# Optimization experiments

Measured on AMD Instinct MI355X. Metric: run time of the kernel, lower is better.

The kernel has to match this reference:

```python
import jax, jax.numpy as jnp
import numpy as np

# NF4 16-level codebook (bitsandbytes values)
NF4_CODEBOOK = jnp.array([
    -1.0, -0.6961928009986877, -0.5250730514526367, -0.39491748809814453,
    -0.28444138169288635, -0.18477343022823334, -0.09105003625154495, 0.0,
    0.07958029955625534, 0.16093020141124725, 0.24611230194568634,
    0.33791524171829224, 0.44070982933044434, 0.5626170039176941,
    0.7229568362236328, 1.0], dtype=jnp.float32)

GROUP = 64      # quant_group_size for NF4
R = 16          # LoRA rank
ALPHA = 16      # lora_alpha -> scaling = ALPHA / R = 1.0
E, H, I, T, TOPK = 8, 2048, 1024, 512, 2


def nf4_dequant_gkn(packed, scales, K, N):
    """packed: [E, K//2, N] uint8-valued ints (two 4-bit codes per byte along K).
    scales: [E, K//GROUP, N] float32 per-group absmax. Returns [E, K, N] fp32."""
    e = packed.shape[0]
    lo = packed & 15
    hi = (packed >> 4) & 15
    codes = jnp.stack([lo, hi], axis=2).reshape(e, K, N)      # interleave along K
    w = NF4_CODEBOOK[codes]                                    # [E, K, N]
    w = w.reshape(e, K // GROUP, GROUP, N) * scales[:, :, None, :]
    return w.reshape(e, K, N)


def setup_inputs() -> dict:
    key = jax.random.key(0)
    ks = jax.random.split(key, 16)
    lora_std = 1.0 / np.sqrt(H)
    return {
        "x": jax.random.normal(ks[0], (T, H), jnp.float32),
        "topk_idx": jax.random.randint(ks[1], (T, TOPK), 0, E, jnp.int32),
        "topk_w": jax.random.uniform(ks[2], (T, TOPK), jnp.float32),
        "gate_packed": jax.random.randint(ks[3], (E, H // 2, I), 0, 256, jnp.int32),
        "gate_scales": jax.random.uniform(ks[4], (E, H // GROUP, I), jnp.float32) * 0.02,
        "up_packed": jax.random.randint(ks[5], (E, H // 2, I), 0, 256, jnp.int32),
        "up_scales": jax.random.uniform(ks[6], (E, H // GROUP, I), jnp.float32) * 0.02,
        "down_packed": jax.random.randint(ks[7], (E, I // 2, H), 0, 256, jnp.int32),
        "down_scales": jax.random.uniform(ks[8], (E, I // GROUP, H), jnp.float32) * 0.02,
        "gate_A": jax.random.normal(ks[9], (E, H, R), jnp.float32) * lora_std,
        "gate_B": jax.random.normal(ks[10], (E, R, I), jnp.float32) * 0.02,
        "up_A": jax.random.normal(ks[11], (E, H, R), jnp.float32) * lora_std,
        "up_B": jax.random.normal(ks[12], (E, R, I), jnp.float32) * 0.02,
        "down_A": jax.random.normal(ks[13], (E, I, R), jnp.float32) * lora_std,
        "down_B": jax.random.normal(ks[14], (E, R, H), jnp.float32) * 0.02,
    }


def reference(x, topk_idx, topk_w, gate_packed, gate_scales, up_packed, up_scales,
              down_packed, down_scales, gate_A, gate_B, up_A, up_B, down_A, down_B):
    scaling = ALPHA / R
    # Dequantized NF4 base + LoRA delta, GKN layout [E, K, N]
    Wg = nf4_dequant_gkn(gate_packed, gate_scales, H, I) + scaling * jnp.einsum('ekr,ern->ekn', gate_A, gate_B)
    Wu = nf4_dequant_gkn(up_packed, up_scales, H, I) + scaling * jnp.einsum('ekr,ern->ekn', up_A, up_B)
    Wd = nf4_dequant_gkn(down_packed, down_scales, I, H) + scaling * jnp.einsum('ekr,ern->ekn', down_A, down_B)
    # Grouped GEMM (dense-over-experts reference): SwiGLU per expert
    g = jnp.einsum('th,ehi->eti', x, Wg)          # [E, T, I]
    u = jnp.einsum('th,ehi->eti', x, Wu)
    h = jax.nn.silu(g) * u
    o = jnp.einsum('eti,eih->eth', h, Wd)         # [E, T, H]
    # Routing combine: per-token per-expert weight from top-k assignments
    w_te = jnp.sum((topk_idx[:, :, None] == jnp.arange(E)) * topk_w[:, :, None], axis=1)  # [T, E]
    return jnp.einsum('eth,te->th', o, w_te)
```

## Files before the change

### kernel.cpp

```cpp
#include <hip/hip_runtime.h>
#include <math.h>

#define NE 8
#define NH 2048
#define NI 1024
#define NT 512
#define NTOPK 2
#define NR 16
#define NGROUP 64
#define NPAIR (NT*NTOPK)

#define SPG 1040
#define SPD 528

typedef short bf16x8 __attribute__((ext_vector_type(8)));
typedef float f32x16 __attribute__((ext_vector_type(16)));
typedef unsigned int u32;

#define MFMA32 __builtin_amdgcn_mfma_f32_32x32x16_bf16

__device__ const float NF4_TAB[16] = {
    -1.0f, -0.6961928009986877f, -0.5250730514526367f, -0.39491748809814453f,
    -0.28444138169288635f, -0.18477343022823334f, -0.09105003625154495f, 0.0f,
    0.07958029955625534f, 0.16093020141124725f, 0.24611230194568634f,
    0.33791524171829224f, 0.44070982933044434f, 0.5626170039176941f,
    0.7229568362236328f, 1.0f};

#define OFF_EXPOFF 0
#define OFF_TOK    256
#define OFF_EXP    4352
#define OFF_W      8448
#define OFF_XAG    12544
#define OFF_XAU    45312
#define OFF_HA     78080
#define OFF_XCT    131072
#define OFF_GU     4325376
#define OFF_HT     10616832
#define OFF_CG     12713984
#define OFF_CU     21233664
#define OFF_CD     29753344

__device__ inline u32 f2bf(float f) {
    return (__float_as_uint(f) + 0x8000u) >> 16;
}
__device__ inline u32 bfpack2(float a, float b) {
    return ((__float_as_uint(a) + 0x8000u) >> 16) |
           ((__float_as_uint(b) + 0x8000u) & 0xFFFF0000u);
}
__device__ inline bf16x8 asbf(uint4 w) {
    union { uint4 u; bf16x8 b; } c; c.u = w; return c.b;
}
__device__ inline bf16x8 bfzero() { return asbf(make_uint4(0,0,0,0)); }
__device__ inline float bf2f(u32 v) { return __uint_as_float(v << 16); }

__device__ __forceinline__ void stage16(const void* g, void* l) {
    __builtin_amdgcn_global_load_lds(
        (const __attribute__((address_space(1))) u32*)g,
        (__attribute__((address_space(3))) u32*)l, 16, 0, 0);
}
#define WAITV0()  asm volatile("s_waitcnt vmcnt(0)" ::: "memory")

__global__ __launch_bounds__(256) void k_cmp3(const u32* __restrict__ gin,
                                              const u32* __restrict__ uin,
                                              const u32* __restrict__ din,
                                              unsigned char* __restrict__ cg,
                                              unsigned char* __restrict__ cu,
                                              unsigned char* __restrict__ cd) {
    __shared__ unsigned char tile[32][33];
    int z = blockIdx.z;
    const u32* in; unsigned char* out; int K2, N, SP, e;
    if (z < 2 * NE) {
        e = z >> 1;
        in = (z & 1) ? uin : gin; out = (z & 1) ? cu : cg;
        K2 = NH / 2; N = NI; SP = SPG;
    } else {
        e = z - 2 * NE;
        in = din; out = cd;
        K2 = NI / 2; N = NH; SP = SPD;
    }
    int kp0 = blockIdx.y * 32, c0 = blockIdx.x * 32;
    if (kp0 >= K2 || c0 >= N) return;
    const u32* ip = in + (size_t)e * K2 * N + (size_t)kp0 * N + c0;
    int tid = threadIdx.x;
    int r = tid >> 5, c = tid & 31;
    #pragma unroll
    for (int i = 0; i < 4; ++i)
        tile[r + 8 * i][c] = (unsigned char)ip[(size_t)(r + 8 * i) * N + c];
    __syncthreads();
    int col = tid >> 3, seg = tid & 7;
    u32 w = (u32)tile[seg * 4 + 0][col] | ((u32)tile[seg * 4 + 1][col] << 8) |
            ((u32)tile[seg * 4 + 2][col] << 16) |
            ((u32)tile[seg * 4 + 3][col] << 24);
    *(u32*)(out + (size_t)e * N * SP + (size_t)(c0 + col) * SP + kp0 + seg * 4) = w;
}

__global__ __launch_bounds__(1024) void k_route(const int* __restrict__ idx,
                                                const float* __restrict__ w,
                                                int* expert_off, int* ptok,
                                                int* pexp, float* pw) {
    __shared__ int cnt[NE], off[NE + 1], cur[NE];
    int tid = threadIdx.x;
    if (tid < NE) cnt[tid] = 0;
    __syncthreads();
    int e = idx[tid];
    float wt = w[tid];
    int t = tid >> 1;
    atomicAdd(&cnt[e], 1);
    __syncthreads();
    if (tid == 0) {
        off[0] = 0;
        for (int i = 0; i < NE; i++) off[i + 1] = off[i] + cnt[i];
    }
    __syncthreads();
    if (tid < NE) cur[tid] = off[tid];
    __syncthreads();
    int pos = atomicAdd(&cur[e], 1);
    ptok[pos] = t; pexp[pos] = e; pw[pos] = wt;
    if (tid <= NE) expert_off[tid] = off[tid];
}

__global__ __launch_bounds__(256) void k_xA(const float* __restrict__ x,
                                            const float* __restrict__ gA,
                                            const float* __restrict__ uA,
                                            const int* __restrict__ ptok,
                                            const int* __restrict__ pexp,
                                            unsigned short* __restrict__ xcT,
                                            unsigned short* __restrict__ xAg,
                                            unsigned short* __restrict__ xAu) {
    __shared__ float xs[NH];
    __shared__ float red[2][64][17];
    int p = blockIdx.x;
    int t = ptok[p], e = pexp[p];
    int tid = threadIdx.x;

    int k = tid * 8;
    const float* xr = x + (size_t)t * NH + k;
    float4 v0 = *(const float4*)xr;
    float4 v1 = *(const float4*)(xr + 4);
    uint4 w;
    w.x = bfpack2(v0.x, v0.y); w.y = bfpack2(v0.z, v0.w);
    w.z = bfpack2(v1.x, v1.y); w.w = bfpack2(v1.z, v1.w);
    *(uint4*)(xcT + ((size_t)(k >> 3) * NPAIR + p) * 8) = w;
    *(float4*)(xs + k) = v0;
    *(float4*)(xs + k + 4) = v1;
    __syncthreads();

    int ch = tid & 63, rg = tid >> 6;
    const float* gAr = gA + (size_t)e * NH * NR + rg * 4;
    const float* uAr = uA + (size_t)e * NH * NR + rg * 4;
    float4 sg = make_float4(0.f, 0.f, 0.f, 0.f);
    float4 su = make_float4(0.f, 0.f, 0.f, 0.f);
    #pragma unroll 4
    for (int jj = 0; jj < NH / 64; ++jj) {
        int j = jj * 64 + ch;
        float xv = xs[j];
        float4 ga = *(const float4*)(gAr + (size_t)j * NR);
        float4 ua = *(const float4*)(uAr + (size_t)j * NR);
        sg.x += xv * ga.x; sg.y += xv * ga.y; sg.z += xv * ga.z; sg.w += xv * ga.w;
        su.x += xv * ua.x; su.y += xv * ua.y; su.z += xv * ua.z; su.w += xv * ua.w;
    }
    red[0][ch][rg * 4 + 0] = sg.x; red[0][ch][rg * 4 + 1] = sg.y;
    red[0][ch][rg * 4 + 2] = sg.z; red[0][ch][rg * 4 + 3] = sg.w;
    red[1][ch][rg * 4 + 0] = su.x; red[1][ch][rg * 4 + 1] = su.y;
    red[1][ch][rg * 4 + 2] = su.z; red[1][ch][rg * 4 + 3] = su.w;
    __syncthreads();
    for (int st = 32; st >= 1; st >>= 1) {
        if (ch < st) {
            #pragma unroll
            for (int i = 0; i < 4; ++i) {
                red[0][ch][rg * 4 + i] += red[0][ch + st][rg * 4 + i];
                red[1][ch][rg * 4 + i] += red[1][ch + st][rg * 4 + i];
            }
        }
        __syncthreads();
    }
    if (tid < 16)
        xAg[p * NR + tid] = (unsigned short)f2bf(red[0][0][tid]);
    else if (tid < 32)
        xAu[p * NR + (tid - 16)] = (unsigned short)f2bf(red[1][0][tid - 16]);
}

__global__ __launch_bounds__(64, 3) void k_gu(
    const unsigned short* __restrict__ xcT,
    const unsigned char* __restrict__ cgp, const float* __restrict__ gsc,
    const unsigned char* __restrict__ cup, const float* __restrict__ usc,
    const float* __restrict__ gB, const float* __restrict__ uB,
    const unsigned short* __restrict__ xAg, const unsigned short* __restrict__ xAu,
    const int* __restrict__ expert_off,
    unsigned short* __restrict__ gu)
{
    __shared__ u32 lut[256];
    __shared__ float sclb[32][32];

    int lane = threadIdx.x;
    int q = lane >> 5, cw = lane & 31;
    for (int i = lane; i < 256; i += 64)
        lut[i] = bfpack2(NF4_TAB[i & 15], NF4_TAB[(i >> 4) & 15]);

    int e = blockIdx.x;
    int c0 = blockIdx.y * 32;
    int mat = blockIdx.z & 1;
    int rt = blockIdx.z >> 1;
    const unsigned char* cp = mat ? cup : cgp;
    const float* scp = mat ? usc : gsc;
    const float* Bp = mat ? uB : gB;
    const unsigned short* xA = mat ? xAu : xAg;

    int off = expert_off[e];
    int cnt = expert_off[e + 1] - off;
    int colg = c0 + cw;

    {
        const float* sg = scp + (size_t)e * (NH / NGROUP) * NI + c0;
        #pragma unroll
        for (int g = 0; g < 4; ++g)
            stage16(sg + (size_t)(g * 8 + (lane >> 3)) * NI + ((lane & 7) << 2),
                    &sclb[g * 8][0]);
    }
    WAITV0();

    const unsigned char* cb = cp + ((size_t)e * NI + colg) * SPG + (q << 4);

    const int NS = NH / 64;
    for (int s0 = rt * 32; s0 < cnt; s0 += 128) {
        int rr = s0 + cw; if (rr > cnt - 1) rr = cnt - 1;
        int prow = off + rr;

        auto loadC = [&](uint4& c, int s) {
            c = *(const uint4*)(cb + (s << 5));
        };
        auto loadA = [&](bf16x8* d, int s) {
            #pragma unroll
            for (int ks = 0; ks < 4; ++ks)
                d[ks] = *(const bf16x8*)(xcT +
                            ((size_t)((s << 3) + (q << 2) + ks) * NPAIR + prow) * 8);
        };

        uint4 C0, C1;
        bf16x8 Aa[4], Ab[4];
        f32x16 acc;
        #pragma unroll
        for (int i = 0; i < 16; ++i) acc[i] = 0.f;

        auto compute = [&](const uint4& cv, const bf16x8* Ar, float scl) {
            const u32* cd = &cv.x;
            f32x16 t;
            #pragma unroll
            for (int i = 0; i < 16; ++i) t[i] = 0.f;
            #pragma unroll
            for (int ks = 0; ks < 4; ++ks) {
                u32 d = cd[ks];
                uint4 w4;
                w4.x = lut[d & 255];
                w4.y = lut[(d >> 8) & 255];
                w4.z = lut[(d >> 16) & 255];
                w4.w = lut[d >> 24];
                t = MFMA32(Ar[ks], asbf(w4), t, 0, 0, 0);
            }
            #pragma unroll
            for (int i = 0; i < 16; ++i) acc[i] += scl * t[i];
        };

        loadC(C0, 0); loadA(Aa, 0);
        loadC(C1, 1); loadA(Ab, 1);
        for (int s = 0; s < NS; s += 2) {
            compute(C0, Aa, sclb[s][cw]);
            if (s + 2 < NS) { loadC(C0, s + 2); loadA(Aa, s + 2); }
            compute(C1, Ab, sclb[s + 1][cw]);
            if (s + 3 < NS) { loadC(C1, s + 3); loadA(Ab, s + 3); }
        }

        {
            bf16x8 la = bfzero();
            if (s0 + cw < cnt)
                la = *(const bf16x8*)(xA + (size_t)(off + s0 + cw) * NR + (q << 3));
            const float* Bq = Bp + ((size_t)e * NR + (q << 3)) * NI + colg;
            uint4 w4; u32* wp = &w4.x;
            #pragma unroll
            for (int i = 0; i < 4; ++i)
                wp[i] = bfpack2(Bq[(2 * i) * NI], Bq[(2 * i + 1) * NI]);
            acc = MFMA32(la, asbf(w4), acc, 0, 0, 0);
        }
        unsigned short* outb = gu + (size_t)mat * NPAIR * NI;
        #pragma unroll
        for (int reg = 0; reg < 16; ++reg) {
            int rloc = (reg & 3) + 8 * (reg >> 2) + (q << 2);
            if (s0 + rloc < cnt)
                outb[(size_t)(off + s0 + rloc) * NI + colg] =
                    (unsigned short)f2bf(acc[reg]);
        }
    }
}

__global__ __launch_bounds__(256) void k_hsw(const unsigned short* __restrict__ gu,
                                             const float* __restrict__ dA,
                                             const int* __restrict__ pexp,
                                             unsigned short* __restrict__ hT,
                                             unsigned short* __restrict__ hA) {
    __shared__ float hs[NI];
    __shared__ float red[64][17];
    int p = blockIdx.x, e = pexp[p];
    int tid = threadIdx.x;

    int i = tid * 4;
    uint2 gv = *(const uint2*)(gu + (size_t)p * NI + i);
    uint2 uv = *(const uint2*)(gu + (size_t)NPAIR * NI + (size_t)p * NI + i);
    const u32* gp = &gv.x; const u32* up = &uv.x;
    uint2 hv; u32* hp = &hv.x;
    float4 h4;
    {
        float g0 = bf2f(gp[0] & 0xFFFFu), g1 = bf2f(gp[0] >> 16);
        float u0 = bf2f(up[0] & 0xFFFFu), u1 = bf2f(up[0] >> 16);
        h4.x = g0 * u0 / (1.f + __expf(-g0));
        h4.y = g1 * u1 / (1.f + __expf(-g1));
        hp[0] = bfpack2(h4.x, h4.y);
        float g2 = bf2f(gp[1] & 0xFFFFu), g3 = bf2f(gp[1] >> 16);
        float u2 = bf2f(up[1] & 0xFFFFu), u3 = bf2f(up[1] >> 16);
        h4.z = g2 * u2 / (1.f + __expf(-g2));
        h4.w = g3 * u3 / (1.f + __expf(-g3));
        hp[1] = bfpack2(h4.z, h4.w);
    }
    *(uint2*)(hT + ((size_t)(i >> 3) * NPAIR + p) * 8 + (i & 7)) = hv;
    *(float4*)(hs + i) = h4;
    __syncthreads();

    int ch = tid & 63, rg = tid >> 6;
    const float* dAr = dA + (size_t)e * NI * NR + rg * 4;
    float4 sv = make_float4(0.f, 0.f, 0.f, 0.f);
    #pragma unroll 4
    for (int jj = 0; jj < NI / 64; ++jj) {
        int j = jj * 64 + ch;
        float hvv = hs[j];
        float4 da = *(const float4*)(dAr + (size_t)j * NR);
        sv.x += hvv * da.x; sv.y += hvv * da.y;
        sv.z += hvv * da.z; sv.w += hvv * da.w;
    }
    red[ch][rg * 4 + 0] = sv.x; red[ch][rg * 4 + 1] = sv.y;
    red[ch][rg * 4 + 2] = sv.z; red[ch][rg * 4 + 3] = sv.w;
    __syncthreads();
    for (int st = 32; st >= 1; st >>= 1) {
        if (ch < st) {
            #pragma unroll
            for (int i2 = 0; i2 < 4; ++i2)
                red[ch][rg * 4 + i2] += red[ch + st][rg * 4 + i2];
        }
        __syncthreads();
    }
    if (tid < 16) hA[p * NR + tid] = (unsigned short)f2bf(red[0][tid]);
}

__global__ __launch_bounds__(64, 3) void k_dn(
    const unsigned short* __restrict__ hT,
    const unsigned char* __restrict__ cdp, const float* __restrict__ dsc,
    const float* __restrict__ dB,
    const unsigned short* __restrict__ hA,
    const int* __restrict__ expert_off, const int* __restrict__ ptok,
    const float* __restrict__ pw,
    float* __restrict__ out)
{
    __shared__ u32 lut[256];
    __shared__ float sclb[16][32];

    int lane = threadIdx.x;
    int q = lane >> 5, cw = lane & 31;
    for (int i = lane; i < 256; i += 64)
        lut[i] = bfpack2(NF4_TAB[i & 15], NF4_TAB[(i >> 4) & 15]);

    int e = blockIdx.x;
    int c0 = blockIdx.y * 32;
    int rt = blockIdx.z;

    int off = expert_off[e];
    int cnt = expert_off[e + 1] - off;
    int colg = c0 + cw;

    {
        const float* sg = dsc + (size_t)e * (NI / NGROUP) * NH + c0;
        #pragma unroll
        for (int g = 0; g < 2; ++g)
            stage16(sg + (size_t)(g * 8 + (lane >> 3)) * NH + ((lane & 7) << 2),
                    &sclb[g * 8][0]);
    }
    WAITV0();

    const unsigned char* cb = cdp + ((size_t)e * NH + colg) * SPD + (q << 4);

    const int NS = NI / 64;
    for (int s0 = rt * 32; s0 < cnt; s0 += 128) {
        int rr = s0 + cw; if (rr > cnt - 1) rr = cnt - 1;
        int prow = off + rr;

        auto loadC = [&](uint4& c, int s) {
            c = *(const uint4*)(cb + (s << 5));
        };
        auto loadA = [&](bf16x8* d, int s) {
            #pragma unroll
            for (int ks = 0; ks < 4; ++ks)
                d[ks] = *(const bf16x8*)(hT +
                            ((size_t)((s << 3) + (q << 2) + ks) * NPAIR + prow) * 8);
        };

        uint4 C0, C1;
        bf16x8 Aa[4], Ab[4];
        f32x16 acc;
        #pragma unroll
        for (int i = 0; i < 16; ++i) acc[i] = 0.f;

        auto compute = [&](const uint4& cv, const bf16x8* Ar, float scl) {
            const u32* cd = &cv.x;
            f32x16 t;
            #pragma unroll
            for (int i = 0; i < 16; ++i) t[i] = 0.f;
            #pragma unroll
            for (int ks = 0; ks < 4; ++ks) {
                u32 d = cd[ks];
                uint4 w4;
                w4.x = lut[d & 255];
                w4.y = lut[(d >> 8) & 255];
                w4.z = lut[(d >> 16) & 255];
                w4.w = lut[d >> 24];
                t = MFMA32(Ar[ks], asbf(w4), t, 0, 0, 0);
            }
            #pragma unroll
            for (int i = 0; i < 16; ++i) acc[i] += scl * t[i];
        };

        loadC(C0, 0); loadA(Aa, 0);
        loadC(C1, 1); loadA(Ab, 1);
        for (int s = 0; s < NS; s += 2) {
            compute(C0, Aa, sclb[s][cw]);
            if (s + 2 < NS) { loadC(C0, s + 2); loadA(Aa, s + 2); }
            compute(C1, Ab, sclb[s + 1][cw]);
            if (s + 3 < NS) { loadC(C1, s + 3); loadA(Ab, s + 3); }
        }

        {
            bf16x8 la = bfzero();
            if (s0 + cw < cnt)
                la = *(const bf16x8*)(hA + (size_t)(off + s0 + cw) * NR + (q << 3));
            const float* Bq = dB + ((size_t)e * NR + (q << 3)) * NH + colg;
            uint4 w4; u32* wp = &w4.x;
            #pragma unroll
            for (int i = 0; i < 4; ++i)
                wp[i] = bfpack2(Bq[(2 * i) * NH], Bq[(2 * i + 1) * NH]);
            acc = MFMA32(la, asbf(w4), acc, 0, 0, 0);
        }
        #pragma unroll
        for (int reg = 0; reg < 16; ++reg) {
            int rloc = (reg & 3) + 8 * (reg >> 2) + (q << 2);
            if (s0 + rloc < cnt) {
                int p = off + s0 + rloc;
                atomicAdd(&out[(size_t)ptok[p] * NH + colg], acc[reg] * pw[p]);
            }
        }
    }
}

extern "C" void kernel_launch(void* const* d_in, const int* in_sizes, int n_in,
                              void* d_out, int out_size, void* d_ws,
                              size_t ws_size, hipStream_t stream) {
    const float* x = (const float*)d_in[0];
    const int* topk_idx = (const int*)d_in[1];
    const float* topk_w = (const float*)d_in[2];
    const int* gate_packed = (const int*)d_in[3];
    const float* gate_scales = (const float*)d_in[4];
    const int* up_packed = (const int*)d_in[5];
    const float* up_scales = (const float*)d_in[6];
    const int* down_packed = (const int*)d_in[7];
    const float* down_scales = (const float*)d_in[8];
    const float* gate_A = (const float*)d_in[9];
    const float* gate_B = (const float*)d_in[10];
    const float* up_A = (const float*)d_in[11];
    const float* up_B = (const float*)d_in[12];
    const float* down_A = (const float*)d_in[13];
    const float* down_B = (const float*)d_in[14];
    float* out = (float*)d_out;

    char* ws = (char*)d_ws;
    int* expert_off = (int*)(ws + OFF_EXPOFF);
    int* ptok = (int*)(ws + OFF_TOK);
    int* pexp = (int*)(ws + OFF_EXP);
    float* pw = (float*)(ws + OFF_W);
    unsigned short* xAg = (unsigned short*)(ws + OFF_XAG);
    unsigned short* xAu = (unsigned short*)(ws + OFF_XAU);
    unsigned short* hA = (unsigned short*)(ws + OFF_HA);
    unsigned short* xcT = (unsigned short*)(ws + OFF_XCT);
    unsigned short* gu = (unsigned short*)(ws + OFF_GU);
    unsigned short* hT = (unsigned short*)(ws + OFF_HT);
    unsigned char* cg = (unsigned char*)(ws + OFF_CG);
    unsigned char* cu = (unsigned char*)(ws + OFF_CU);
    unsigned char* cd = (unsigned char*)(ws + OFF_CD);

    hipMemsetAsync(d_out, 0, (size_t)NT * NH * sizeof(float), stream);

    k_cmp3<<<dim3(NH / 32, (NH / 2) / 32, 3 * NE), 256, 0, stream>>>(
        (const u32*)gate_packed, (const u32*)up_packed, (const u32*)down_packed,
        cg, cu, cd);

    k_route<<<1, 1024, 0, stream>>>(topk_idx, topk_w, expert_off, ptok, pexp, pw);
    k_xA<<<NPAIR, 256, 0, stream>>>(x, gate_A, up_A, ptok, pexp, xcT, xAg, xAu);
    k_gu<<<dim3(NE, NI / 32, 8), 64, 0, stream>>>(
        xcT, cg, gate_scales, cu, up_scales, gate_B, up_B,
        xAg, xAu, expert_off, gu);
    k_hsw<<<NPAIR, 256, 0, stream>>>(gu, down_A, pexp, hT, hA);
    k_dn<<<dim3(NE, NH / 32, 4), 64, 0, stream>>>(
        hT, cd, down_scales, down_B, hA, expert_off, ptok, pw, out);
}
```

Baseline: 265.7 us.

## Widen NF4 repack tiles with vector loads/stores and fold routing into repack kernel

The byte-repack kernel now has each block cover 128 columns instead of 32. Each thread reads packed weights with 16-byte vector loads, packs them into 32-bit words in shared memory, and writes 16-byte vector stores. Routing (counting, prefix offsets, pair scatter) moves into one extra z-slice of the same launch, so the separate k_route kernel and its launch overhead go away. The aim is to cut memory-transaction count and launch count in the preprocessing stage. The cost is more complex indexing and one lightly loaded routing block running alongside the repack blocks.

```diff
diff --git a/kernel.cpp b/kernel.cpp
--- a/kernel.cpp
+++ b/kernel.cpp
@@ -65,58 +65,84 @@
                                               const u32* __restrict__ din,
                                               unsigned char* __restrict__ cg,
                                               unsigned char* __restrict__ cu,
-                                              unsigned char* __restrict__ cd) {
-    __shared__ unsigned char tile[32][33];
+                                              unsigned char* __restrict__ cd,
+                                              const int* __restrict__ idx,
+                                              const float* __restrict__ w,
+                                              int* expert_off, int* ptok,
+                                              int* pexp, float* pw) {
+    __shared__ u32 tile32[32][33];
+    __shared__ int cnt[NE], off2[NE + 1], cur[NE];
+    int tid = threadIdx.x;
     int z = blockIdx.z;
+
+    if (z == 24) {
+        if (blockIdx.x || blockIdx.y) return;
+        if (tid < NE) cnt[tid] = 0;
+        __syncthreads();
+        int e4[4]; float w4[4];
+        #pragma unroll
+        for (int i = 0; i < 4; ++i) {
+            int pr = tid * 4 + i;
+            e4[i] = idx[pr]; w4[i] = w[pr];
+            atomicAdd(&cnt[e4[i]], 1);
+        }
+        __syncthreads();
+        if (tid == 0) {
+            off2[0] = 0;
+            for (int i = 0; i < NE; i++) off2[i + 1] = off2[i] + cnt[i];
+        }
+        __syncthreads();
+        if (tid < NE) cur[tid] = off2[tid];
+        __syncthreads();
+        #pragma unroll
+        for (int i = 0; i < 4; ++i) {
+            int pr = tid * 4 + i;
+            int pos = atomicAdd(&cur[e4[i]], 1);
+            ptok[pos] = pr >> 1; pexp[pos] = e4[i]; pw[pos] = w4[i];
+        }
+        if (tid <= NE) expert_off[tid] = off2[tid];
+        return;
+    }
+
     const u32* in; unsigned char* out; int K2, N, SP, e;
     if (z < 2 * NE) {
         e = z >> 1;
         in = (z & 1) ? uin : gin; out = (z & 1) ? cu : cg;
         K2 = NH / 2; N = NI; SP = SPG;
+        if ((int)blockIdx.x >= N / 128) return;
     } else {
         e = z - 2 * NE;
         in = din; out = cd;
         K2 = NI / 2; N = NH; SP = SPD;
-    }
-    int kp0 = blockIdx.y * 32, c0 = blockIdx.x * 32;
-    if (kp0 >= K2 || c0 >= N) return;
+        if ((int)blockIdx.y >= K2 / 32) return;
+    }
+    int kp0 = blockIdx.y * 32, c0 = blockIdx.x * 128;
+
+    int c16 = tid & 31, rr = tid >> 5;
     const u32* ip = in + (size_t)e * K2 * N + (size_t)kp0 * N + c0;
-    int tid = threadIdx.x;
-    int r = tid >> 5, c = tid & 31;
     #pragma unroll
-    for (int i = 0; i < 4; ++i)
-        tile[r + 8 * i][c] = (unsigned char)ip[(size_t)(r + 8 * i) * N + c];
+    for (int pass = 0; pass < 4; ++pass) {
+        int r = pass * 8 + rr;
+        uint4 v = *(const uint4*)(ip + (size_t)r * N + c16 * 4);
+        tile32[r][c16] = (v.x & 255) | ((v.y & 255) << 8) |
+                         ((v.z & 255) << 16) | ((v.w & 255) << 24);
+    }
     __syncthreads();
-    int col = tid >> 3, seg = tid & 7;
-    u32 w = (u32)tile[seg * 4 + 0][col] | ((u32)tile[seg * 4 + 1][col] << 8) |
-            ((u32)tile[seg * 4 + 2][col] << 16) |
-            ((u32)tile[seg * 4 + 3][col] << 24);
-    *(u32*)(out + (size_t)e * N * SP + (size_t)(c0 + col) * SP + kp0 + seg * 4) = w;
-}
-
-__global__ __launch_bounds__(1024) void k_route(const int* __restrict__ idx,
-                                                const float* __restrict__ w,
-                                                int* expert_off, int* ptok,
-                                                int* pexp, float* pw) {
-    __shared__ int cnt[NE], off[NE + 1], cur[NE];
-    int tid = threadIdx.x;
-    if (tid < NE) cnt[tid] = 0;
-    __syncthreads();
-    int e = idx[tid];
-    float wt = w[tid];
-    int t = tid >> 1;
-    atomicAdd(&cnt[e], 1);
-    __syncthreads();
-    if (tid == 0) {
-        off[0] = 0;
-        for (int i = 0; i < NE; i++) off[i + 1] = off[i] + cnt[i];
-    }
-    __syncthreads();
-    if (tid < NE) cur[tid] = off[tid];
-    __syncthreads();
-    int pos = atomicAdd(&cur[e], 1);
-    ptok[pos] = t; pexp[pos] = e; pw[pos] = wt;
-    if (tid <= NE) expert_off[tid] = off[tid];
+
+    int col = tid >> 1, half = tid & 1;
+    int cq = col >> 2, sh = (col & 3) * 8;
+    uint4 ow; u32* op = &ow.x;
+    #pragma unroll
+    for (int i = 0; i < 4; ++i) {
+        int base = half * 16 + i * 4;
+        u32 b0 = (tile32[base + 0][cq] >> sh) & 255;
+        u32 b1 = (tile32[base + 1][cq] >> sh) & 255;
+        u32 b2 = (tile32[base + 2][cq] >> sh) & 255;
+        u32 b3 = (tile32[base + 3][cq] >> sh) & 255;
+        op[i] = b0 | (b1 << 8) | (b2 << 16) | (b3 << 24);
+    }
+    *(uint4*)(out + (size_t)e * N * SP + (size_t)(c0 + col) * SP
+              + kp0 + half * 16) = ow;
 }
 
 __global__ __launch_bounds__(256) void k_xA(const float* __restrict__ x,
@@ -493,11 +519,10 @@
 
     hipMemsetAsync(d_out, 0, (size_t)NT * NH * sizeof(float), stream);
 
-    k_cmp3<<<dim3(NH / 32, (NH / 2) / 32, 3 * NE), 256, 0, stream>>>(
+    k_cmp3<<<dim3(16, 32, 25), 256, 0, stream>>>(
         (const u32*)gate_packed, (const u32*)up_packed, (const u32*)down_packed,
-        cg, cu, cd);
-
-    k_route<<<1, 1024, 0, stream>>>(topk_idx, topk_w, expert_off, ptok, pexp, pw);
+        cg, cu, cd, topk_idx, topk_w, expert_off, ptok, pexp, pw);
+
     k_xA<<<NPAIR, 256, 0, stream>>>(x, gate_A, up_A, ptok, pexp, xcT, xAg, xAu);
     k_gu<<<dim3(NE, NI / 32, 8), 64, 0, stream>>>(
         xcT, cg, gate_scales, cu, up_scales, gate_B, up_B,
```

New measurement: 271.1 us. +2.0%, slower.
